# Kernel tuning notes

Hardware: AMD Instinct MI355X
Metric: run time of the kernel (lower is better)

Reference implementation:

```python
import jax, jax.numpy as jnp
import numpy as np

NUM_WIRES = 14
N_LAYERS = 3


def setup_inputs() -> dict:
    key = jax.random.key(0)
    k1, k2, k3, k4, k5 = jax.random.split(key, 5)
    B, D = 1024, 2 ** NUM_WIRES
    sr = jax.random.normal(k1, (B, D), dtype=jnp.float32)
    si = jax.random.normal(k2, (B, D), dtype=jnp.float32)
    # normalize each complex state vector (StatePreparation requires unit norm)
    norm = jnp.sqrt(jnp.sum(sr * sr + si * si, axis=-1, keepdims=True))
    sr, si = sr / norm, si / norm
    var_params = jax.random.normal(k3, (N_LAYERS, NUM_WIRES, 3), dtype=jnp.float32)
    head_w = jax.random.normal(k4, (1, NUM_WIRES), dtype=jnp.float32) / np.sqrt(NUM_WIRES)
    head_b = jax.random.normal(k5, (1,), dtype=jnp.float32) * 0.01
    return {"state_real": sr, "state_imag": si, "var_params": var_params,
            "head_w": head_w, "head_b": head_b}


def _apply_1q(psi, U, w):
    # psi: (B, 2, 2, ..., 2); wire w lives on axis 1+w (wire 0 = MSB, PennyLane order)
    psi = jnp.moveaxis(psi, 1 + w, -1)
    psi = jnp.einsum('ij,...j->...i', U, psi)
    return jnp.moveaxis(psi, -1, 1 + w)


def _apply_cnot(psi, c, t):
    psi = jnp.moveaxis(psi, (1 + c, 1 + t), (-2, -1))
    psi = jnp.stack([psi[..., 0, :], psi[..., 1, ::-1]], axis=-2)
    return jnp.moveaxis(psi, (-2, -1), (1 + c, 1 + t))


def _rot_matrix(theta_x, theta_y, theta_z):
    # combined RZ @ RY @ RX (RX applied first), complex64 2x2
    cx, sx = jnp.cos(theta_x / 2), jnp.sin(theta_x / 2)
    cy, sy = jnp.cos(theta_y / 2), jnp.sin(theta_y / 2)
    RX = jnp.array([[cx, -1j * sx], [-1j * sx, cx]], dtype=jnp.complex64)
    RY = jnp.array([[cy, -sy], [sy, cy]], dtype=jnp.complex64)
    ez = jnp.exp(-1j * theta_z.astype(jnp.complex64) / 2)
    RZ = jnp.array([[1.0, 0.0], [0.0, 0.0]], dtype=jnp.complex64) * ez + \
         jnp.array([[0.0, 0.0], [0.0, 1.0]], dtype=jnp.complex64) * jnp.conj(ez)
    return RZ @ RY @ RX


def reference(state_real, state_imag, var_params, head_w, head_b):
    B = state_real.shape[0]
    n = NUM_WIRES
    psi = (state_real + 1j * state_imag).astype(jnp.complex64)
    psi = psi.reshape((B,) + (2,) * n)
    for l in range(N_LAYERS):
        for w in range(n):
            U = _rot_matrix(var_params[l, w, 0], var_params[l, w, 1], var_params[l, w, 2])
            psi = _apply_1q(psi, U, w)
        for w in range(n - 1):
            psi = _apply_cnot(psi, w, w + 1)
        psi = _apply_cnot(psi, n - 1, 0)
    probs = jnp.real(psi * jnp.conj(psi))  # (B, 2, ..., 2)
    feats = []
    all_axes = tuple(range(1, n + 1))
    for w in range(n):
        other = tuple(a for a in all_axes if a != 1 + w)
        m = jnp.sum(probs, axis=other)  # (B, 2)
        feats.append(m[:, 0] - m[:, 1])  # <Z_w>
    features = jnp.stack(feats, axis=-1).astype(jnp.float32)  # (B, num_wires)
    out = features @ head_w.T + head_b  # (B, 1)
    return out.squeeze(-1)
```

## Files before the change

kernel.cpp:

```cpp
#include <hip/hip_runtime.h>

#define NW 14
#define NL 3
#define NGAT 42
#define DIM 16384
#define BLOCK 1024


typedef float        f4  __attribute__((ext_vector_type(4)));
typedef _Float16     h8  __attribute__((ext_vector_type(8)));
typedef unsigned int u4v __attribute__((ext_vector_type(4)));

constexpr int parity14(int v) { int p = 0; for (int i = 0; i < NW; ++i) p ^= (v >> i) & 1; return p; }
constexpr int hibit(int v) { int h = -1; for (int i = 0; i < NW; ++i) if ((v >> i) & 1) h = i; return h; }

struct Lin { int col[NW]; };

constexpr int lin_apply(const Lin& M, int x) {
    int r = 0;
    for (int i = 0; i < NW; ++i) if ((x >> i) & 1) r ^= M.col[i];
    return r;
}
constexpr Lin lin_inverse(const Lin& M) {
    int E[NW] = {}, P[NW] = {};
    for (int i = 0; i < NW; ++i) {
        int v = M.col[i], p = 1 << i;
        while (v) {
            int h = hibit(v);
            if (!E[h]) { E[h] = v; P[h] = p; break; }
            v ^= E[h]; p ^= P[h];
        }
    }
    Lin R{};
    for (int i = 0; i < NW; ++i) {
        int v = 1 << i, p = 0;
        while (v) { int h = hibit(v); v ^= E[h]; p ^= P[h]; }
        R.col[i] = p;
    }
    return R;
}
constexpr Lin lin_compose(const Lin& A, const Lin& B) {
    Lin R{};
    for (int i = 0; i < NW; ++i) R.col[i] = lin_apply(A, B.col[i]);
    return R;
}

struct Alg {
    int ngates[12];
    int gidx[12][4];
    int basisA[12][4];
    int comboA[12][16];
    int cvecA[12][10];
    Lin F[12];
    int Rf[NW];
};

constexpr Alg make_alg() {
    Alg A{};
    int R[NW] = {}, C[NW] = {};
    for (int p = 0; p < NW; ++p) { R[p] = 1 << p; C[p] = 1 << p; }
    int bi = 0;
    for (int l = 0; l < NL; ++l) {
        const int sizes[4] = {4, 4, 4, 2};
        int w0 = 0;
        for (int s = 0; s < 4; ++s) {
            const int ng = sizes[s];
            A.ngates[bi] = ng;
            int basis[4] = {}, rr[4] = {};
            for (int j = 0; j < ng; ++j) {
                int w = w0 + j, p = 13 - w;
                basis[j] = C[p];
                rr[j] = R[p];
                A.gidx[bi][j] = l * NW + w;
            }
            int ech[4] = {}; int ne = 0;
            for (int j = 0; j < ng; ++j) {
                int v = basis[j];
                bool ch = true;
                while (ch) { ch = false;
                    for (int k = 0; k < ne; ++k)
                        if (v && ((v >> hibit(ech[k])) & 1)) { v ^= ech[k]; ch = true; }
                }
                ech[ne++] = v;
            }
            int nb = ng;
            for (int cand = 1; cand < DIM && nb < 4; ++cand) {
                bool ok = true;
                for (int j = 0; j < ng; ++j) if (parity14(cand & rr[j])) { ok = false; break; }
                if (!ok) continue;
                int v = cand;
                bool ch = true;
                while (ch) { ch = false;
                    for (int k = 0; k < ne; ++k)
                        if (v && ((v >> hibit(ech[k])) & 1)) { v ^= ech[k]; ch = true; }
                }
                if (v) { basis[nb++] = cand; ech[ne++] = v; }
            }
            int piv[4] = {};
            for (int k = 0; k < 4; ++k) piv[k] = hibit(ech[k]);
            for (int a = 0; a < 4; ++a)
                for (int b2 = a + 1; b2 < 4; ++b2)
                    if (piv[b2] < piv[a]) { int t = piv[a]; piv[a] = piv[b2]; piv[b2] = t; }
            int npp[10] = {}; int nn = 0;
            for (int bit = 0; bit < NW; ++bit) {
                bool isp = false;
                for (int k = 0; k < 4; ++k) if (piv[k] == bit) isp = true;
                if (!isp) npp[nn++] = bit;
            }
            for (int k = 0; k < 10; ++k) {
                int c = 1 << npp[k];
                for (int j = 0; j < ng; ++j) if ((rr[j] >> npp[k]) & 1) c ^= basis[j];
                A.cvecA[bi][k] = c;
            }
            for (int e = 0; e < 16; ++e) {
                int v = 0;
                for (int j = 0; j < 4; ++j) if ((e >> j) & 1) v ^= basis[j];
                A.comboA[bi][e] = v;
            }
            for (int j = 0; j < 4; ++j) A.basisA[bi][j] = basis[j];
            for (int j = 0; j < 4; ++j) A.F[bi].col[j] = basis[j];
            for (int k = 0; k < 10; ++k) A.F[bi].col[4 + k] = A.cvecA[bi][k];
            w0 += ng;
            ++bi;
        }
        for (int w = 0; w < NW; ++w) {
            int c = w, t = (w + 1) % NW;
            int pc = 13 - c, pt = 13 - t;
            R[pt] ^= R[pc];
            C[pc] ^= C[pt];
        }
    }
    for (int p = 0; p < NW; ++p) A.Rf[p] = R[p];
    return A;
}

struct Twist { unsigned t[10]; };

constexpr int rankv(const int* v, int nv, int width) {
    int basis[8] = {};
    int rk = 0;
    for (int i = 0; i < nv; ++i) {
        int x = v[i] & ((1 << width) - 1);
        for (int b = width - 1; b >= 0; --b) {
            if (!((x >> b) & 1)) continue;
            if (basis[b]) { x ^= basis[b]; continue; }
            basis[b] = x; ++rk; break;
        }
    }
    return rk;
}

constexpr int img5(int u, const unsigned* t) {
    int r = u & 31;
    for (int k = 0; k < 10; ++k) if ((u >> (4 + k)) & 1) r ^= (int)t[k];
    return r;
}

constexpr int eval5(const unsigned* t, const int (*preR)[5], const int* preS) {
    {
        int w[4] = { 4 ^ (int)((t[0] >> 2) & 7), (int)((t[1] >> 2) & 7),
                     (int)((t[2] >> 2) & 7), (int)((t[3] >> 2) & 7) };
        if (rankv(w, 4, 3) < 3) return -1;
    }
    int sc = 0;
    for (int r = 1; r < 12; ++r) {
        int v[5];
        for (int i = 0; i < 5; ++i) v[i] = img5(preR[r][i], t);
        sc += rankv(v, 5, 5);
    }
    {
        int v[5];
        for (int i = 0; i < 5; ++i) v[i] = img5(preS[i], t);
        sc += rankv(v, 5, 5);
    }
    return sc;
}

constexpr Twist find_twist() {
    Alg A = make_alg();
    int preR[12][5] = {};
    for (int r = 1; r < 12; ++r) {
        Lin Fi = lin_inverse(A.F[r - 1]);
        for (int k = 0; k < 4; ++k) preR[r][k] = lin_apply(Fi, A.cvecA[r][k]);
        preR[r][4] = lin_apply(Fi, A.basisA[r][2]);
    }
    int preS[5] = {};
    {
        Lin F0i = lin_inverse(A.F[0]);
        for (int k = 0; k < 5; ++k) preS[k] = lin_apply(F0i, 1 << (k + 2));
    }
    Twist best{};
    for (int k = 0; k < 10; ++k) best.t[k] = 0;
    int bs = eval5(best.t, preR, preS);
    unsigned x = 0x9E3779B9u;
    for (int s = 0; s < 2; ++s) {
        Twist cur{};
        if (s == 0) {
            for (int k = 0; k < 10; ++k) cur.t[k] = 0;
        } else {
            for (int k = 0; k < 10; ++k) {
                x = x * 1664525u + 1013904223u;
                const unsigned m = (k == 0) ? 3u : 7u;
                cur.t[k] = ((x >> 13) & m) << 2;
            }
        }
        int cs = eval5(cur.t, preR, preS);
        for (int pass = 0; pass < 2; ++pass) {
            for (int k = 0; k < 10; ++k) {
                unsigned bc = cur.t[k];
                int bv = cs;
                const unsigned lim = (k == 0) ? 16u : 32u;
                for (unsigned c = 0; c < lim; c += 4) {
                    cur.t[k] = c;
                    const int e = eval5(cur.t, preR, preS);
                    if (e > bv) { bv = e; bc = c; }
                }
                cur.t[k] = bc;
                cs = bv;
            }
        }
        if (cs > bs) { bs = cs; best = cur; }
    }
    return best;
}

constexpr Twist TW = find_twist();

struct BatchP {
    int ngates;
    int gidx[4];
    unsigned rdy[10];
    unsigned rde[16];
};
struct PlanP {
    BatchP b[12];
    unsigned stB[14];
    unsigned ykey[14];
    int zsel[14];
    unsigned tw[10];
};

constexpr PlanP make_planp() {
    Alg A = make_alg();
    PlanP P{};
    for (int bi = 0; bi < 12; ++bi) {
        P.b[bi].ngates = A.ngates[bi];
        for (int j = 0; j < 4; ++j) P.b[bi].gidx[j] = A.gidx[bi][j];
    }
    Lin T{};
    for (int j = 0; j < 4; ++j) T.col[j] = 1 << j;
    for (int k = 0; k < 10; ++k) T.col[4 + k] = (1 << (4 + k)) ^ (int)TW.t[k];

    {
        Lin L0 = lin_compose(T, lin_inverse(A.F[0]));
        for (int bit = 0; bit < NW; ++bit) P.stB[bit] = (unsigned)lin_apply(L0, 1 << bit) * 4u;
    }
    for (int r = 1; r < 12; ++r) {
        Lin Lw = lin_compose(T, lin_inverse(A.F[r - 1]));
        for (int k = 0; k < 10; ++k) P.b[r].rdy[k] = (unsigned)lin_apply(Lw, A.cvecA[r][k]) * 4u;
        for (int e = 0; e < 16; ++e) P.b[r].rde[e] = (unsigned)lin_apply(Lw, A.comboA[r][e]) * 4u;
    }
    for (int w = 0; w < NW; ++w) {
        int zrw = A.Rf[13 - w];
        unsigned ym = 0;
        for (int k = 0; k < 10; ++k) ym |= (unsigned)parity14(A.cvecA[11][k] & zrw) << k;
        int qm = parity14(A.basisA[11][2] & zrw) | (parity14(A.basisA[11][3] & zrw) << 1);
        P.ykey[w] = ym | ((unsigned)qm << 10);
        P.zsel[w] = parity14(A.basisA[11][0] & zrw) | (parity14(A.basisA[11][1] & zrw) << 1);
    }
    for (int k = 0; k < 10; ++k) P.tw[k] = TW.t[k];
    return P;
}

constexpr PlanP PL = make_planp();

constexpr unsigned TILE_OFF[4] = {
    0u,
    (1u << 10) ^ (PL.tw[4] << 2),
    (1u << 11) ^ (PL.tw[5] << 2),
    (1u << 10) ^ (1u << 11) ^ ((PL.tw[4] ^ PL.tw[5]) << 2)
};

__device__ __forceinline__ unsigned pk_rn(float r, float i) {
    const unsigned hr = (unsigned)__builtin_bit_cast(unsigned short, (_Float16)r);
    const unsigned hi = (unsigned)__builtin_bit_cast(unsigned short, (_Float16)i);
    return hr | (hi << 16);
}
__device__ __forceinline__ float2 up(unsigned d) {
    float2 c;
    c.x = (float)__builtin_bit_cast(_Float16, (unsigned short)(d & 0xffffu));
    c.y = (float)__builtin_bit_cast(_Float16, (unsigned short)(d >> 16));
    return c;
}

__device__ __forceinline__ f4 mfh(u4v a, u4v b, f4 c) {
    return __builtin_amdgcn_mfma_f32_16x16x32_f16(
        __builtin_bit_cast(h8, a), __builtin_bit_cast(h8, b), c, 0, 0, 0);
}

#define RD_SREP(B)                                                     \
    unsigned srep = 0;                                                 \
    srep ^= (n & 1u)   ? B.rdy[0] : 0u;                                \
    srep ^= (n & 2u)   ? B.rdy[1] : 0u;                                \
    srep ^= (n & 4u)   ? B.rdy[2] : 0u;                                \
    srep ^= (n & 8u)   ? B.rdy[3] : 0u;                                \
    srep ^= (wid & 1u) ? B.rdy[6] : 0u;                                \
    srep ^= (wid & 2u) ? B.rdy[7] : 0u;                                \
    srep ^= (wid & 4u) ? B.rdy[8] : 0u;                                \
    srep ^= (wid & 8u) ? B.rdy[9] : 0u;                                \
    srep ^= (q & 1u)   ? B.rde[4] : 0u;                                \
    srep ^= (q & 2u)   ? B.rde[8] : 0u;

template <int BI>
__device__ __forceinline__ void mfma_batch(char* __restrict__ lds, const float* __restrict__ gm,
                                           unsigned* __restrict__ atab, const unsigned bnq) {
    constexpr BatchP B = PL.b[BI];
    const unsigned tid = threadIdx.x;
    const unsigned lane = tid & 63u, wid = tid >> 6;
    const unsigned n = lane & 15u, q = lane >> 4;

    __syncthreads();

    if (tid < 256) {
        const unsigned m = tid >> 4, ein = tid & 15u;
        float wr = 1.f, wi = 0.f;
        #pragma unroll
        for (int j = 0; j < 4; ++j) {
            if (j < B.ngates) {
                const unsigned mj = (m >> j) & 1u, ej = (ein >> j) & 1u;
                const float ur = gm[B.gidx[j] * 8 + (int)(mj * 4u + ej * 2u)];
                const float ui = gm[B.gidx[j] * 8 + (int)(mj * 4u + ej * 2u) + 1];
                const float nr = wr * ur - wi * ui;
                const float ni = wr * ui + wi * ur;
                wr = nr; wi = ni;
            }
        }
        if (B.ngates < 4 && (((m ^ ein) >> B.ngates) != 0u)) { wr = 0.f; wi = 0.f; }
        const unsigned o = m * 16u + (ein ^ (m & 12u));
        atab[o]        = pk_rn(wr, -wi);
        atab[256 + o]  = pk_rn(wi, wr);
    }

    u4v bfr[4];
    if constexpr (BI == 0) {
        #pragma unroll
        for (int t = 0; t < 4; ++t) {
            bfr[t] = *(const u4v*)(lds + (bnq ^ TILE_OFF[t]));
        }
    } else {
        RD_SREP(B)
        #pragma unroll
        for (int t = 0; t < 4; ++t) {
            const unsigned st = srep ^ ((t & 1) ? B.rdy[4] : 0u) ^ ((t & 2) ? B.rdy[5] : 0u);
            const unsigned c0 = *(const unsigned*)(lds + st);
            const unsigned c1 = *(const unsigned*)(lds + (st ^ B.rde[1]));
            const unsigned c2 = *(const unsigned*)(lds + (st ^ B.rde[2]));
            const unsigned c3 = *(const unsigned*)(lds + (st ^ B.rde[3]));
            u4v v; v.x = c0; v.y = c1; v.z = c2; v.w = c3;
            bfr[t] = v;
        }
    }

    __syncthreads();

    const unsigned tix = (n << 4) + (((q << 2) ^ (n & 12u)));
    const u4v A0 = *(const u4v*)&atab[tix];
    const u4v A1 = *(const u4v*)&atab[256 + tix];

    #pragma unroll
    for (int t = 0; t < 4; ++t) {
        f4 ar = {0.f, 0.f, 0.f, 0.f};
        f4 ai = {0.f, 0.f, 0.f, 0.f};
        ar = mfh(A0, bfr[t], ar);
        ai = mfh(A1, bfr[t], ai);
        u4v s;
        s.x = pk_rn(ar.x, ai.x);
        s.y = pk_rn(ar.y, ai.y);
        s.z = pk_rn(ar.z, ai.z);
        s.w = pk_rn(ar.w, ai.w);
        *(u4v*)(lds + (bnq ^ TILE_OFF[t])) = s;
    }
}

#define BFC(A, B_, ua, ub) { const float2 t0 = A, t1 = B_; \
    A.x  = ua.x * t0.x - ua.y * t0.y + ua.z * t1.x - ua.w * t1.y; \
    A.y  = ua.x * t0.y + ua.y * t0.x + ua.z * t1.y + ua.w * t1.x; \
    B_.x = ub.x * t0.x - ub.y * t0.y + ub.z * t1.x - ub.w * t1.y; \
    B_.y = ub.x * t0.y + ub.y * t0.x + ub.z * t1.y + ub.w * t1.x; }

__device__ __forceinline__ float tail_batch(char* __restrict__ lds, const float* __restrict__ gm,
                                            const float* __restrict__ g_hw) {
    constexpr BatchP B = PL.b[11];
    const unsigned tid = threadIdx.x;
    const unsigned lane = tid & 63u, wid = tid >> 6;
    const unsigned n = lane & 15u, q = lane >> 4;
    __syncthreads();
    const f4 u0a = *(const f4*)&gm[B.gidx[0] * 8];
    const f4 u0b = *(const f4*)&gm[B.gidx[0] * 8 + 4];
    const f4 u1a = *(const f4*)&gm[B.gidx[1] * 8];
    const f4 u1b = *(const f4*)&gm[B.gidx[1] * 8 + 4];
    float hwv[NW];
    #pragma unroll
    for (int w = 0; w < NW; ++w) hwv[w] = g_hw[w];
    float acc = 0.f;
    RD_SREP(B)
    #pragma unroll
    for (int t = 0; t < 4; ++t) {
        const unsigned st = srep ^ ((t & 1) ? B.rdy[4] : 0u) ^ ((t & 2) ? B.rdy[5] : 0u);
        float2 c0 = up(*(const unsigned*)(lds + st));
        float2 c1 = up(*(const unsigned*)(lds + (st ^ B.rde[1])));
        float2 c2 = up(*(const unsigned*)(lds + (st ^ B.rde[2])));
        float2 c3 = up(*(const unsigned*)(lds + (st ^ B.rde[3])));
        BFC(c0, c1, u0a, u0b)  BFC(c2, c3, u0a, u0b)
        BFC(c0, c2, u1a, u1b)  BFC(c1, c3, u1a, u1b)
        const float p0 = c0.x * c0.x + c0.y * c0.y;
        const float p1 = c1.x * c1.x + c1.y * c1.y;
        const float p2 = c2.x * c2.x + c2.y * c2.y;
        const float p3 = c3.x * c3.x + c3.y * c3.y;
        const float sa = p0 + p1, sb = p0 - p1, sc = p2 + p3, sd = p2 - p3;
        const float W4[4] = {sa + sc, sb + sd, sa - sc, sb - sd};
        const unsigned y = (wid << 6) | ((unsigned)t << 4) | n;
        const unsigned key = y | (q << 10);
        #pragma unroll
        for (int w = 0; w < NW; ++w) {
            const unsigned sg = ((unsigned)__popc(key & PL.ykey[w])) << 31;
            const float s = __uint_as_float(__float_as_uint(hwv[w]) ^ sg);
            acc += W4[PL.zsel[w]] * s;
        }
    }
    return acc;
}

__global__ __launch_bounds__(BLOCK, 8) void qsim_kernel(
    const float* __restrict__ g_sr, const float* __restrict__ g_si,
    const float* __restrict__ g_params, const float* __restrict__ g_hw,
    const float* __restrict__ g_hb, float* __restrict__ g_out)
{
    extern __shared__ char lds[];
    __shared__ __align__(16) float gm[NGAT * 8];
    __shared__ __align__(16) unsigned atab[512];
    __shared__ float red[BLOCK / 64];

    const unsigned tid = threadIdx.x;
    const int b = blockIdx.x;
    const float* __restrict__ srcr = g_sr + (size_t)b * DIM;
    const float* __restrict__ srci = g_si + (size_t)b * DIM;

    if (tid < NGAT) {
        const float tx = g_params[tid * 3 + 0];
        const float ty = g_params[tid * 3 + 1];
        const float tz = g_params[tid * 3 + 2];
        const float cx = cosf(0.5f * tx), sx = sinf(0.5f * tx);
        const float cy = cosf(0.5f * ty), sy = sinf(0.5f * ty);
        const float cz = cosf(0.5f * tz), sz = sinf(0.5f * tz);
        const float a00r = cy * cx,  a00i = sy * sx;
        const float a01r = -sy * cx, a01i = -cy * sx;
        const float a10r = sy * cx,  a10i = -cy * sx;
        const float a11r = cy * cx,  a11i = -sy * sx;
        gm[tid * 8 + 0] = cz * a00r + sz * a00i;
        gm[tid * 8 + 1] = cz * a00i - sz * a00r;
        gm[tid * 8 + 2] = cz * a01r + sz * a01i;
        gm[tid * 8 + 3] = cz * a01i - sz * a01r;
        gm[tid * 8 + 4] = cz * a10r - sz * a10i;
        gm[tid * 8 + 5] = cz * a10i + sz * a10r;
        gm[tid * 8 + 6] = cz * a11r - sz * a11i;
        gm[tid * 8 + 7] = cz * a11i + sz * a11r;
    }

    const unsigned lane0 = tid & 63u, wid0 = tid >> 6;
    const unsigned n0 = lane0 & 15u, q0 = lane0 >> 4;
    unsigned twv = 0;
    #pragma unroll
    for (int k = 0; k < 4; ++k) twv ^= ((n0 >> k) & 1u) ? PL.tw[k] : 0u;
    #pragma unroll
    for (int k = 0; k < 4; ++k) twv ^= ((wid0 >> k) & 1u) ? PL.tw[6 + k] : 0u;
    const unsigned bnq = ((wid0 << 10) ^ (n0 << 4) ^ (q0 << 2) ^ twv) << 2;

    unsigned bb = 0;
    #pragma unroll
    for (int k = 0; k < 10; ++k) bb ^= ((tid >> k) & 1u) ? PL.stB[k + 2] : 0u;
    #pragma unroll
    for (int it = 0; it < 4; ++it) {
        const int x = (int)tid * 4 + it * 4096;
        const f4 r4 = *(const f4*)(srcr + x);
        const f4 i4 = *(const f4*)(srci + x);
        const unsigned base = bb ^ ((it & 1) ? PL.stB[12] : 0u) ^ ((it & 2) ? PL.stB[13] : 0u);
        *(unsigned*)(lds + base) = pk_rn(r4.x, i4.x);
        *(unsigned*)(lds + (base ^ PL.stB[0])) = pk_rn(r4.y, i4.y);
        *(unsigned*)(lds + (base ^ PL.stB[1])) = pk_rn(r4.z, i4.z);
        *(unsigned*)(lds + (base ^ (PL.stB[0] ^ PL.stB[1]))) = pk_rn(r4.w, i4.w);
    }

    mfma_batch<0>(lds, gm, atab, bnq);
    mfma_batch<1>(lds, gm, atab, bnq);
    mfma_batch<2>(lds, gm, atab, bnq);
    mfma_batch<3>(lds, gm, atab, bnq);
    mfma_batch<4>(lds, gm, atab, bnq);
    mfma_batch<5>(lds, gm, atab, bnq);
    mfma_batch<6>(lds, gm, atab, bnq);
    mfma_batch<7>(lds, gm, atab, bnq);
    mfma_batch<8>(lds, gm, atab, bnq);
    mfma_batch<9>(lds, gm, atab, bnq);
    mfma_batch<10>(lds, gm, atab, bnq);

    float acc = tail_batch(lds, gm, g_hw);

    #pragma unroll
    for (int off = 32; off > 0; off >>= 1) acc += __shfl_down(acc, off);
    const int lane = tid & 63, wid = tid >> 6;
    if (lane == 0) red[wid] = acc;
    __syncthreads();
    if (tid == 0) {
        float s = 0.0f;
        #pragma unroll
        for (int k = 0; k < BLOCK / 64; ++k) s += red[k];
        g_out[b] = s + g_hb[0];
    }
}

extern "C" void kernel_launch(void* const* d_in, const int* in_sizes, int n_in,
                              void* d_out, int out_size, void* d_ws, size_t ws_size,
                              hipStream_t stream) {
    const float* sr = (const float*)d_in[0];
    const float* si = (const float*)d_in[1];
    const float* vp = (const float*)d_in[2];
    const float* hw = (const float*)d_in[3];
    const float* hb = (const float*)d_in[4];
    float* out = (float*)d_out;

    dim3 grid(out_size);
    dim3 block(BLOCK);
    size_t shmem = (size_t)DIM * 4;
    qsim_kernel<<<grid, block, shmem, stream>>>(sr, si, vp, hw, hb, out);
}
```

Measured before the change: 190.9 us.

## Fuse first two gate batches into one register-resident MFMA pair

The first two 4-gate batches (wires 0-3 and 4-7) are merged into one pass. Each 16x16 tile is multiplied by the first gate matrix on the right and the second on the left, so the intermediate result stays in registers. This removes one LDS write/read round trip and two block barriers. The initial state layout and the batch-2 read permutation are replanned at compile time to fit, and the gate table in shared memory is doubled.

```diff
diff --git a/kernel.cpp b/kernel.cpp
--- a/kernel.cpp
+++ b/kernel.cpp
@@ -134,6 +134,23 @@
     return A;
 }
 
+constexpr Lin make_fin() {
+    Lin F{};
+    for (int j = 0; j < 4; ++j) F.col[j]     = 1 << (13 - j);
+    for (int j = 0; j < 4; ++j) F.col[4 + j] = 1 << (9 - j);
+    for (int k = 0; k < 6; ++k) F.col[8 + k] = 1 << (5 - k);
+    return F;
+}
+constexpr Lin make_fp0() {
+    Lin F{};
+    for (int j = 0; j < 4; ++j) F.col[j]     = 1 << (9 - j);
+    for (int j = 0; j < 4; ++j) F.col[4 + j] = 1 << (13 - j);
+    for (int k = 0; k < 6; ++k) F.col[8 + k] = 1 << (5 - k);
+    return F;
+}
+constexpr Lin FIN = make_fin();
+constexpr Lin FP0 = make_fp0();
+
 struct Twist { unsigned t[10]; };
 
 constexpr int rankv(const int* v, int nv, int width) {
@@ -163,7 +180,7 @@
         if (rankv(w, 4, 3) < 3) return -1;
     }
     int sc = 0;
-    for (int r = 1; r < 12; ++r) {
+    for (int r = 2; r < 12; ++r) {
         int v[5];
         for (int i = 0; i < 5; ++i) v[i] = img5(preR[r][i], t);
         sc += rankv(v, 5, 5);
@@ -179,14 +196,15 @@
 constexpr Twist find_twist() {
     Alg A = make_alg();
     int preR[12][5] = {};
-    for (int r = 1; r < 12; ++r) {
-        Lin Fi = lin_inverse(A.F[r - 1]);
+    for (int r = 2; r < 12; ++r) {
+        Lin Fprev = (r == 2) ? FP0 : A.F[r - 1];
+        Lin Fi = lin_inverse(Fprev);
         for (int k = 0; k < 4; ++k) preR[r][k] = lin_apply(Fi, A.cvecA[r][k]);
         preR[r][4] = lin_apply(Fi, A.basisA[r][2]);
     }
     int preS[5] = {};
     {
-        Lin F0i = lin_inverse(A.F[0]);
+        Lin F0i = lin_inverse(FIN);
         for (int k = 0; k < 5; ++k) preS[k] = lin_apply(F0i, 1 << (k + 2));
     }
     Twist best{};
@@ -252,11 +270,12 @@
     for (int k = 0; k < 10; ++k) T.col[4 + k] = (1 << (4 + k)) ^ (int)TW.t[k];
 
     {
-        Lin L0 = lin_compose(T, lin_inverse(A.F[0]));
+        Lin L0 = lin_compose(T, lin_inverse(FIN));
         for (int bit = 0; bit < NW; ++bit) P.stB[bit] = (unsigned)lin_apply(L0, 1 << bit) * 4u;
     }
-    for (int r = 1; r < 12; ++r) {
-        Lin Lw = lin_compose(T, lin_inverse(A.F[r - 1]));
+    for (int r = 2; r < 12; ++r) {
+        Lin Fprev = (r == 2) ? FP0 : A.F[r - 1];
+        Lin Lw = lin_compose(T, lin_inverse(Fprev));
         for (int k = 0; k < 10; ++k) P.b[r].rdy[k] = (unsigned)lin_apply(Lw, A.cvecA[r][k]) * 4u;
         for (int e = 0; e < 16; ++e) P.b[r].rde[e] = (unsigned)lin_apply(Lw, A.comboA[r][e]) * 4u;
     }
@@ -311,6 +330,72 @@
     srep ^= (q & 1u)   ? B.rde[4] : 0u;                                \
     srep ^= (q & 2u)   ? B.rde[8] : 0u;
 
+__device__ __forceinline__ void mfma_pair0(char* __restrict__ lds, const float* __restrict__ gm,
+                                           unsigned* __restrict__ atab, const unsigned bnq) {
+    const unsigned tid = threadIdx.x;
+    const unsigned lane = tid & 63u, wid = tid >> 6;
+    const unsigned n = lane & 15u, q = lane >> 4;
+
+    __syncthreads();
+
+    if (tid < 512) {
+        const unsigned idx = tid & 255u;
+        const unsigned m = idx >> 4, ein = idx & 15u;
+        const int gbase = (tid < 256) ? 0 : 4;
+        float wr = 1.f, wi = 0.f;
+        #pragma unroll
+        for (int j = 0; j < 4; ++j) {
+            const unsigned mj = (m >> j) & 1u, ej = (ein >> j) & 1u;
+            const float ur = gm[(gbase + j) * 8 + (int)(mj * 4u + ej * 2u)];
+            const float ui = gm[(gbase + j) * 8 + (int)(mj * 4u + ej * 2u) + 1];
+            const float nr = wr * ur - wi * ui;
+            const float ni = wr * ui + wi * ur;
+            wr = nr; wi = ni;
+        }
+        const unsigned o = m * 16u + (ein ^ (m & 12u));
+        unsigned* __restrict__ tab = atab + ((tid < 256) ? 0 : 512);
+        tab[o]        = pk_rn(wr, -wi);
+        tab[256 + o]  = pk_rn(wi, wr);
+    }
+
+    u4v bfr[4];
+    #pragma unroll
+    for (int t = 0; t < 4; ++t) {
+        bfr[t] = *(const u4v*)(lds + (bnq ^ TILE_OFF[t]));
+    }
+
+    __syncthreads();
+
+    const unsigned tix = (n << 4) + (((q << 2) ^ (n & 12u)));
+    const u4v War = *(const u4v*)&atab[tix];
+    const u4v Wai = *(const u4v*)&atab[256 + tix];
+    const u4v Wbr = *(const u4v*)&atab[512 + tix];
+    const u4v Wbi = *(const u4v*)&atab[768 + tix];
+
+    #pragma unroll
+    for (int t = 0; t < 4; ++t) {
+        f4 dr = {0.f, 0.f, 0.f, 0.f};
+        f4 di = {0.f, 0.f, 0.f, 0.f};
+        dr = mfh(bfr[t], War, dr);
+        di = mfh(bfr[t], Wai, di);
+        u4v pb;
+        pb.x = pk_rn(dr.x, di.x);
+        pb.y = pk_rn(dr.y, di.y);
+        pb.z = pk_rn(dr.z, di.z);
+        pb.w = pk_rn(dr.w, di.w);
+        f4 ar = {0.f, 0.f, 0.f, 0.f};
+        f4 ai = {0.f, 0.f, 0.f, 0.f};
+        ar = mfh(Wbr, pb, ar);
+        ai = mfh(Wbi, pb, ai);
+        u4v s;
+        s.x = pk_rn(ar.x, ai.x);
+        s.y = pk_rn(ar.y, ai.y);
+        s.z = pk_rn(ar.z, ai.z);
+        s.w = pk_rn(ar.w, ai.w);
+        *(u4v*)(lds + (bnq ^ TILE_OFF[t])) = s;
+    }
+}
+
 template <int BI>
 __device__ __forceinline__ void mfma_batch(char* __restrict__ lds, const float* __restrict__ gm,
                                            unsigned* __restrict__ atab, const unsigned bnq) {
@@ -342,12 +427,7 @@
     }
 
     u4v bfr[4];
-    if constexpr (BI == 0) {
-        #pragma unroll
-        for (int t = 0; t < 4; ++t) {
-            bfr[t] = *(const u4v*)(lds + (bnq ^ TILE_OFF[t]));
-        }
-    } else {
+    {
         RD_SREP(B)
         #pragma unroll
         for (int t = 0; t < 4; ++t) {
@@ -438,7 +518,7 @@
 {
     extern __shared__ char lds[];
     __shared__ __align__(16) float gm[NGAT * 8];
-    __shared__ __align__(16) unsigned atab[512];
+    __shared__ __align__(16) unsigned atab[1024];
     __shared__ float red[BLOCK / 64];
 
     const unsigned tid = threadIdx.x;
@@ -491,8 +571,7 @@
         *(unsigned*)(lds + (base ^ (PL.stB[0] ^ PL.stB[1]))) = pk_rn(r4.w, i4.w);
     }
 
-    mfma_batch<0>(lds, gm, atab, bnq);
-    mfma_batch<1>(lds, gm, atab, bnq);
+    mfma_pair0(lds, gm, atab, bnq);
     mfma_batch<2>(lds, gm, atab, bnq);
     mfma_batch<3>(lds, gm, atab, bnq);
     mfma_batch<4>(lds, gm, atab, bnq);
```

Result: faster. 186.8 us (-2.1%).
